# Kernel tuning notes

Measured on AMD Instinct MI355X. Metric: run time of the kernel, lower is better.

## Reference

```python
import jax, jax.numpy as jnp
import numpy as np

B, I, H = 4096, 1024, 1024


def setup_inputs() -> dict:
    key = jax.random.key(0)
    ks = jax.random.split(key, 22)
    def n(k, shape, scale=1.0):
        return jax.random.normal(k, shape, dtype=jnp.float32) * scale
    s = 0.02  # small init for weights to keep gates in sensitive range
    return {
        "x": n(ks[0], (B, I)),
        "h": n(ks[1], (B, H)),
        "c": n(ks[2], (B, H)),
        "W_ii_w": n(ks[3], (H, I), s), "W_ii_b": n(ks[4], (H,), s),
        "W_hi_w": n(ks[5], (H, H), s), "W_hi_b": n(ks[6], (H,), s),
        "W_ci":   n(ks[7], (H,), s),
        "W_if_w": n(ks[8], (H, I), s), "W_if_b": n(ks[9], (H,), s),
        "W_hf_w": n(ks[10], (H, H), s), "W_hf_b": n(ks[11], (H,), s),
        "W_cf":   n(ks[12], (H,), s),
        "W_ig_w": n(ks[13], (H, I), s), "W_ig_b": n(ks[14], (H,), s),
        "W_hg_w": n(ks[15], (H, H), s), "W_hg_b": n(ks[16], (H,), s),
        "W_io_w": n(ks[17], (H, I), s), "W_io_b": n(ks[18], (H,), s),
        "W_ho_w": n(ks[19], (H, H), s), "W_ho_b": n(ks[20], (H,), s),
        "W_co":   n(ks[21], (H,), s),
    }


def reference(x, h, c,
              W_ii_w, W_ii_b, W_hi_w, W_hi_b, W_ci,
              W_if_w, W_if_b, W_hf_w, W_hf_b, W_cf,
              W_ig_w, W_ig_b, W_hg_w, W_hg_b,
              W_io_w, W_io_b, W_ho_w, W_ho_b, W_co):
    # Fuse the 4 input projections and 4 hidden projections into single GEMMs.
    # Weight layout matches torch nn.Linear: y = x @ W.T + b
    Wx = jnp.concatenate([W_ii_w, W_if_w, W_ig_w, W_io_w], axis=0)  # [4H, I]
    Wh = jnp.concatenate([W_hi_w, W_hf_w, W_hg_w, W_ho_w], axis=0)  # [4H, H]
    bx = jnp.concatenate([W_ii_b, W_if_b, W_ig_b, W_io_b])          # [4H]
    bh = jnp.concatenate([W_hi_b, W_hf_b, W_hg_b, W_ho_b])          # [4H]
    z = x @ Wx.T + h @ Wh.T + (bx + bh)  # [B, 4H]
    zi, zf, zg, zo = jnp.split(z, 4, axis=-1)
    i = jax.nn.sigmoid(zi + W_ci * c)
    f = jax.nn.sigmoid(zf + W_cf * c)
    g = jnp.tanh(zg)
    c_next = f * c + i * g
    o = jax.nn.sigmoid(zo + W_co * c_next)
    h_next = o * jnp.tanh(c_next)
    return (h_next, c_next)
```

## Files before the change

kernel.cpp:

```cpp
#include <hip/hip_runtime.h>
#include <hip/hip_bf16.h>

#define BD 4096
#define ID 1024
#define HD 1024
#define KD 2048
#define ND 4096

typedef __attribute__((ext_vector_type(8))) __bf16 bf16x8;
typedef __attribute__((ext_vector_type(4))) float f32x4;

static __device__ __forceinline__ unsigned short f2bf(float f) {
  union { float f; unsigned u; } v; v.f = f;
  unsigned u = v.u;
  unsigned r = u + 0x7fffu + ((u >> 16) & 1u);
  return (unsigned short)(r >> 16);
}
static __device__ __forceinline__ float bf2f(unsigned short s) {
  union { unsigned u; float f; } v; v.u = ((unsigned)s) << 16;
  return v.f;
}

static __device__ __forceinline__ void gload_lds16(const void* g, void* l) {
  __builtin_amdgcn_global_load_lds(
      (const __attribute__((address_space(1))) void*)g,
      (__attribute__((address_space(3))) void*)l, 16, 0, 0);
}

static __device__ __forceinline__ float fast_sigmoid(float x) {
  return 1.0f / (1.0f + __expf(-x));
}
static __device__ __forceinline__ float fast_tanh(float x) {
  float t = __expf(-2.0f * fabsf(x));
  float r = (1.0f - t) / (1.0f + t);
  return copysignf(r, x);
}

__global__ void pack_AB(const float* __restrict__ x, const float* __restrict__ h,
                        const float* __restrict__ wxi, const float* __restrict__ wxf,
                        const float* __restrict__ wxg, const float* __restrict__ wxo,
                        const float* __restrict__ whi, const float* __restrict__ whf,
                        const float* __restrict__ whg, const float* __restrict__ who,
                        unsigned short* __restrict__ A, unsigned short* __restrict__ Bm) {
  if (blockIdx.x < 8192) {
    int idx = blockIdx.x * blockDim.x + threadIdx.x;
    int e = idx << 2;
    int b = e >> 11;
    int k = e & 2047;
    const float* src = (k < ID) ? (x + (size_t)b * ID + k)
                                : (h + (size_t)b * HD + (k - ID));
    float4 v = *reinterpret_cast<const float4*>(src);
    ushort4 o;
    o.x = f2bf(v.x); o.y = f2bf(v.y); o.z = f2bf(v.z); o.w = f2bf(v.w);
    *reinterpret_cast<ushort4*>(A + e) = o;
  } else {
    int idx = (blockIdx.x - 8192) * blockDim.x + threadIdx.x;
    int e = idx << 2;
    int n = e >> 11;
    int k = e & 2047;
    int g = n >> 10, r = n & 1023;
    const float* src;
    if (k < ID) {
      src = (g == 0) ? wxi : (g == 1) ? wxf : (g == 2) ? wxg : wxo;
      src += (size_t)r * ID + k;
    } else {
      src = (g == 0) ? whi : (g == 1) ? whf : (g == 2) ? whg : who;
      src += (size_t)r * HD + (k - ID);
    }
    float4 v = *reinterpret_cast<const float4*>(src);
    ushort4 o;
    o.x = f2bf(v.x); o.y = f2bf(v.y); o.z = f2bf(v.z); o.w = f2bf(v.w);
    *reinterpret_cast<ushort4*>(Bm + e) = o;
  }
}

__global__ __launch_bounds__(512, 2) void gemm_bf16(
    const unsigned short* __restrict__ A,
    const unsigned short* __restrict__ Bm,
    unsigned short* __restrict__ Z) {
  __shared__ __attribute__((aligned(16))) unsigned short lds[65536];

  const int tid  = threadIdx.x;
  const int lane = tid & 63;
  const int w    = tid >> 6;
  const int wr   = w >> 2;
  const int wc   = w & 3;

  const int bid = blockIdx.x;
  const int swz = (bid & 7) * 32 + (bid >> 3);
  const int m0  = (swz >> 4) * 256;
  const int n0  = (swz & 15) * 256;

  f32x4 acc[8][4];
#pragma unroll
  for (int i = 0; i < 8; ++i)
#pragma unroll
    for (int j = 0; j < 4; ++j)
      acc[i][j] = (f32x4){0.f, 0.f, 0.f, 0.f};

  const int sw  = lane & 7;
  const int rA0 = (wr * 128 + (lane & 15)) * 64;
  const int rB0 = (wc * 64  + (lane & 15)) * 64;
  const int offk0 = (((lane >> 4)    ) ^ sw) * 8;
  const int offk1 = (((lane >> 4) + 4) ^ sw) * 8;

  unsigned short* ldsA = lds;
  unsigned short* ldsB = lds + 32768;

  auto stage = [&](int buf, int kt) {
#pragma unroll
    for (int j = 0; j < 4; ++j) {
      int ci  = j * 512 + tid;
      int row = ci >> 3;
      int sc  = (ci & 7) ^ (row & 7);
      const unsigned short* gA = A  + (size_t)(m0 + row) * KD + kt + sc * 8;
      const unsigned short* gB = Bm + (size_t)(n0 + row) * KD + kt + sc * 8;
      unsigned short* lA = ldsA + buf * 16384 + (j * 512 + (tid & ~63)) * 8;
      unsigned short* lB = ldsB + buf * 16384 + (j * 512 + (tid & ~63)) * 8;
      gload_lds16(gA, lA);
      gload_lds16(gB, lB);
    }
  };

  stage(0, 0);

  for (int T = 0; T < 32; ++T) {
    const int buf = T & 1;
    const unsigned short* pA = ldsA + buf * 16384;
    const unsigned short* pB = ldsB + buf * 16384;

    asm volatile("s_waitcnt vmcnt(0)" ::: "memory");
    __builtin_amdgcn_s_barrier();
    __builtin_amdgcn_sched_barrier(0);

    bf16x8 bfr[4][2];
#pragma unroll
    for (int ni = 0; ni < 4; ++ni) {
      bfr[ni][0] = *(const bf16x8*)(pB + rB0 + ni * 1024 + offk0);
      bfr[ni][1] = *(const bf16x8*)(pB + rB0 + ni * 1024 + offk1);
    }

    if (T < 31) stage(buf ^ 1, (T + 1) * 64);
    __builtin_amdgcn_sched_barrier(0);

#pragma unroll
    for (int p = 0; p < 4; ++p) {
      bf16x8 af[2][2];
#pragma unroll
      for (int i = 0; i < 2; ++i) {
        af[i][0] = *(const bf16x8*)(pA + rA0 + (2 * p + i) * 1024 + offk0);
        af[i][1] = *(const bf16x8*)(pA + rA0 + (2 * p + i) * 1024 + offk1);
      }
      __builtin_amdgcn_s_setprio(1);
#pragma unroll
      for (int i = 0; i < 2; ++i)
#pragma unroll
        for (int ni = 0; ni < 4; ++ni)
#pragma unroll
          for (int kk = 0; kk < 2; ++kk)
            acc[2 * p + i][ni] = __builtin_amdgcn_mfma_f32_16x16x32_bf16(
                af[i][kk], bfr[ni][kk], acc[2 * p + i][ni], 0, 0, 0);
      __builtin_amdgcn_s_setprio(0);
      __builtin_amdgcn_s_barrier();
    }
  }

  const int col0 = n0 + wc * 64 + (lane & 15);
  const int row0 = m0 + wr * 128 + (lane >> 4) * 4;
#pragma unroll
  for (int mi = 0; mi < 8; ++mi)
#pragma unroll
    for (int ni = 0; ni < 4; ++ni)
#pragma unroll
      for (int q = 0; q < 4; ++q)
        Z[(size_t)(row0 + mi * 16 + q) * ND + col0 + ni * 16] =
            f2bf(acc[mi][ni][q]);
}

__global__ void lstm_cell(const unsigned short* __restrict__ Z,
                          const float* __restrict__ c,
                          const float* __restrict__ bxi, const float* __restrict__ bhi,
                          const float* __restrict__ bxf, const float* __restrict__ bhf,
                          const float* __restrict__ bxg, const float* __restrict__ bhg,
                          const float* __restrict__ bxo, const float* __restrict__ bho,
                          const float* __restrict__ pci, const float* __restrict__ pcf,
                          const float* __restrict__ pco,
                          float* __restrict__ out) {
  int idx = blockIdx.x * blockDim.x + threadIdx.x;
  int e = idx << 2;
  int b = e >> 10;
  int r = e & 1023;
  const size_t zrow = (size_t)b * ND;

  ushort4 zi4 = *(const ushort4*)&Z[zrow + r];
  ushort4 zf4 = *(const ushort4*)&Z[zrow + 1024 + r];
  ushort4 zg4 = *(const ushort4*)&Z[zrow + 2048 + r];
  ushort4 zo4 = *(const ushort4*)&Z[zrow + 3072 + r];
  float4 c4   = *(const float4*)&c[e];
  float4 vbxi = *(const float4*)&bxi[r];
  float4 vbhi = *(const float4*)&bhi[r];
  float4 vbxf = *(const float4*)&bxf[r];
  float4 vbhf = *(const float4*)&bhf[r];
  float4 vbxg = *(const float4*)&bxg[r];
  float4 vbhg = *(const float4*)&bhg[r];
  float4 vbxo = *(const float4*)&bxo[r];
  float4 vbho = *(const float4*)&bho[r];
  float4 vpci = *(const float4*)&pci[r];
  float4 vpcf = *(const float4*)&pcf[r];
  float4 vpco = *(const float4*)&pco[r];

  unsigned short ziu[4] = {zi4.x, zi4.y, zi4.z, zi4.w};
  unsigned short zfu[4] = {zf4.x, zf4.y, zf4.z, zf4.w};
  unsigned short zgu[4] = {zg4.x, zg4.y, zg4.z, zg4.w};
  unsigned short zou[4] = {zo4.x, zo4.y, zo4.z, zo4.w};
  float cc[4]  = {c4.x, c4.y, c4.z, c4.w};
  float bi_[4] = {vbxi.x + vbhi.x, vbxi.y + vbhi.y, vbxi.z + vbhi.z, vbxi.w + vbhi.w};
  float bf_[4] = {vbxf.x + vbhf.x, vbxf.y + vbhf.y, vbxf.z + vbhf.z, vbxf.w + vbhf.w};
  float bg_[4] = {vbxg.x + vbhg.x, vbxg.y + vbhg.y, vbxg.z + vbhg.z, vbxg.w + vbhg.w};
  float bo_[4] = {vbxo.x + vbho.x, vbxo.y + vbho.y, vbxo.z + vbho.z, vbxo.w + vbho.w};
  float pi_[4] = {vpci.x, vpci.y, vpci.z, vpci.w};
  float pf_[4] = {vpcf.x, vpcf.y, vpcf.z, vpcf.w};
  float po_[4] = {vpco.x, vpco.y, vpco.z, vpco.w};

  float hn[4], cn[4];
#pragma unroll
  for (int j = 0; j < 4; ++j) {
    float vi = bf2f(ziu[j]) + bi_[j] + pi_[j] * cc[j];
    float vf = bf2f(zfu[j]) + bf_[j] + pf_[j] * cc[j];
    float vg = bf2f(zgu[j]) + bg_[j];
    float vo = bf2f(zou[j]) + bo_[j];
    float ig = fast_sigmoid(vi);
    float fg = fast_sigmoid(vf);
    float gg = fast_tanh(vg);
    float cnext = fg * cc[j] + ig * gg;
    float og = fast_sigmoid(vo + po_[j] * cnext);
    cn[j] = cnext;
    hn[j] = og * fast_tanh(cnext);
  }
  float4 ho = {hn[0], hn[1], hn[2], hn[3]};
  float4 co = {cn[0], cn[1], cn[2], cn[3]};
  *(float4*)&out[e] = ho;
  *(float4*)&out[(size_t)BD * HD + e] = co;
}

extern "C" void kernel_launch(void* const* d_in, const int* in_sizes, int n_in,
                              void* d_out, int out_size, void* d_ws, size_t ws_size,
                              hipStream_t stream) {
  const float* x      = (const float*)d_in[0];
  const float* h      = (const float*)d_in[1];
  const float* c      = (const float*)d_in[2];
  const float* W_ii_w = (const float*)d_in[3];
  const float* W_ii_b = (const float*)d_in[4];
  const float* W_hi_w = (const float*)d_in[5];
  const float* W_hi_b = (const float*)d_in[6];
  const float* W_ci   = (const float*)d_in[7];
  const float* W_if_w = (const float*)d_in[8];
  const float* W_if_b = (const float*)d_in[9];
  const float* W_hf_w = (const float*)d_in[10];
  const float* W_hf_b = (const float*)d_in[11];
  const float* W_cf   = (const float*)d_in[12];
  const float* W_ig_w = (const float*)d_in[13];
  const float* W_ig_b = (const float*)d_in[14];
  const float* W_hg_w = (const float*)d_in[15];
  const float* W_hg_b = (const float*)d_in[16];
  const float* W_io_w = (const float*)d_in[17];
  const float* W_io_b = (const float*)d_in[18];
  const float* W_ho_w = (const float*)d_in[19];
  const float* W_ho_b = (const float*)d_in[20];
  const float* W_co   = (const float*)d_in[21];

  unsigned short* Apack = (unsigned short*)d_ws;
  unsigned short* Bpack = Apack + (size_t)BD * KD;
  unsigned short* Zbuf  = Bpack + (size_t)ND * KD;
  float* out = (float*)d_out;

  pack_AB<<<dim3(16384), dim3(256), 0, stream>>>(
      x, h, W_ii_w, W_if_w, W_ig_w, W_io_w, W_hi_w, W_hf_w, W_hg_w, W_ho_w,
      Apack, Bpack);
  gemm_bf16<<<dim3(256), dim3(512), 0, stream>>>(Apack, Bpack, Zbuf);
  lstm_cell<<<dim3(4096), dim3(256), 0, stream>>>(Zbuf, c,
      W_ii_b, W_hi_b, W_if_b, W_hf_b, W_ig_b, W_hg_b, W_io_b, W_ho_b,
      W_ci, W_cf, W_co, out);
}
```

Measured before the change: 234.9 us.

## Split A-tile staging per sub-phase and wait on partial vmcnt counts

Global-to-LDS loads for the next A tile are now split into four row chunks, one issued per sub-phase p of the compute loop, while B is issued at p==0. Each sub-phase waits only on the vmcnt needed for its A chunk, replacing the full vmcnt(0) drain at the top of each K step. The last K step is peeled into an epilogue with a decreasing vmcnt countdown. The goal is to spread memory issue across the MFMA work and shorten stalls. The trade-off is more barriers, plus correctness that depends on exact per-thread load counts and the LDS layout matching the reader indexing.

Result: no change. 234.1 us (-0.3%).

```diff
diff --git a/kernel.cpp b/kernel.cpp
--- a/kernel.cpp
+++ b/kernel.cpp
@@ -107,50 +107,62 @@
   unsigned short* ldsA = lds;
   unsigned short* ldsB = lds + 32768;
 
-  auto stage = [&](int buf, int kt) {
-#pragma unroll
-    for (int j = 0; j < 4; ++j) {
-      int ci  = j * 512 + tid;
+  auto stageB = [&](int buf, int kt) {
+#pragma unroll
+    for (int q = 0; q < 4; ++q) {
+      int ci  = q * 512 + tid;
       int row = ci >> 3;
       int sc  = (ci & 7) ^ (row & 7);
-      const unsigned short* gA = A  + (size_t)(m0 + row) * KD + kt + sc * 8;
-      const unsigned short* gB = Bm + (size_t)(n0 + row) * KD + kt + sc * 8;
-      unsigned short* lA = ldsA + buf * 16384 + (j * 512 + (tid & ~63)) * 8;
-      unsigned short* lB = ldsB + buf * 16384 + (j * 512 + (tid & ~63)) * 8;
-      gload_lds16(gA, lA);
-      gload_lds16(gB, lB);
+      gload_lds16(Bm + (size_t)(n0 + row) * KD + kt + sc * 8,
+                  ldsB + buf * 16384 + (q * 512 + w * 64) * 8);
     }
   };
-
-  stage(0, 0);
-
-  for (int T = 0; T < 32; ++T) {
+  auto stageA = [&](int buf, int kt, int p) {
+    int half = tid >> 8;
+    int idx  = tid & 255;
+    int row  = half * 128 + p * 32 + (idx >> 3);
+    int sc   = (idx & 7) ^ ((idx >> 3) & 7);
+    gload_lds16(A + (size_t)(m0 + row) * KD + kt + sc * 8,
+                ldsA + buf * 16384 + (half * 1024 + p * 256 + (w & 3) * 64) * 8);
+  };
+
+  stageB(0, 0);
+  stageA(0, 0, 0);
+  stageA(0, 0, 1);
+  stageA(0, 0, 2);
+  stageA(0, 0, 3);
+
+  bf16x8 bfr[4][2];
+
+  for (int T = 0; T < 31; ++T) {
     const int buf = T & 1;
     const unsigned short* pA = ldsA + buf * 16384;
     const unsigned short* pB = ldsB + buf * 16384;
-
-    asm volatile("s_waitcnt vmcnt(0)" ::: "memory");
+    const int ktn = (T + 1) * 64;
+
+    asm volatile("s_waitcnt vmcnt(3)" ::: "memory");
     __builtin_amdgcn_s_barrier();
     __builtin_amdgcn_sched_barrier(0);
 
-    bf16x8 bfr[4][2];
-#pragma unroll
-    for (int ni = 0; ni < 4; ++ni) {
-      bfr[ni][0] = *(const bf16x8*)(pB + rB0 + ni * 1024 + offk0);
-      bfr[ni][1] = *(const bf16x8*)(pB + rB0 + ni * 1024 + offk1);
-    }
-
-    if (T < 31) stage(buf ^ 1, (T + 1) * 64);
-    __builtin_amdgcn_sched_barrier(0);
-
 #pragma unroll
     for (int p = 0; p < 4; ++p) {
+      if (p == 0) {
+#pragma unroll
+        for (int ni = 0; ni < 4; ++ni) {
+          bfr[ni][0] = *(const bf16x8*)(pB + rB0 + ni * 1024 + offk0);
+          bfr[ni][1] = *(const bf16x8*)(pB + rB0 + ni * 1024 + offk1);
+        }
+      }
       bf16x8 af[2][2];
 #pragma unroll
       for (int i = 0; i < 2; ++i) {
         af[i][0] = *(const bf16x8*)(pA + rA0 + (2 * p + i) * 1024 + offk0);
         af[i][1] = *(const bf16x8*)(pA + rA0 + (2 * p + i) * 1024 + offk1);
       }
+      if (p == 0) { stageB(buf ^ 1, ktn); stageA(buf ^ 1, ktn, 0); }
+      else        { stageA(buf ^ 1, ktn, p); }
+      __builtin_amdgcn_sched_barrier(0);
+
       __builtin_amdgcn_s_setprio(1);
 #pragma unroll
       for (int i = 0; i < 2; ++i)
@@ -161,7 +173,51 @@
             acc[2 * p + i][ni] = __builtin_amdgcn_mfma_f32_16x16x32_bf16(
                 af[i][kk], bfr[ni][kk], acc[2 * p + i][ni], 0, 0, 0);
       __builtin_amdgcn_s_setprio(0);
-      __builtin_amdgcn_s_barrier();
+
+      if (p < 3) {
+        asm volatile("s_waitcnt vmcnt(7)" ::: "memory");
+        __builtin_amdgcn_s_barrier();
+      }
+    }
+  }
+
+  {
+    const unsigned short* pA = ldsA + 16384;
+    const unsigned short* pB = ldsB + 16384;
+
+    asm volatile("s_waitcnt vmcnt(3)" ::: "memory");
+    __builtin_amdgcn_s_barrier();
+    __builtin_amdgcn_sched_barrier(0);
+
+#pragma unroll
+    for (int p = 0; p < 4; ++p) {
+      if (p == 0) {
+#pragma unroll
+        for (int ni = 0; ni < 4; ++ni) {
+          bfr[ni][0] = *(const bf16x8*)(pB + rB0 + ni * 1024 + offk0);
+          bfr[ni][1] = *(const bf16x8*)(pB + rB0 + ni * 1024 + offk1);
+        }
+      }
+      bf16x8 af[2][2];
+#pragma unroll
+      for (int i = 0; i < 2; ++i) {
+        af[i][0] = *(const bf16x8*)(pA + rA0 + (2 * p + i) * 1024 + offk0);
+        af[i][1] = *(const bf16x8*)(pA + rA0 + (2 * p + i) * 1024 + offk1);
+      }
+      __builtin_amdgcn_s_setprio(1);
+#pragma unroll
+      for (int i = 0; i < 2; ++i)
+#pragma unroll
+        for (int ni = 0; ni < 4; ++ni)
+#pragma unroll
+          for (int kk = 0; kk < 2; ++kk)
+            acc[2 * p + i][ni] = __builtin_amdgcn_mfma_f32_16x16x32_bf16(
+                af[i][kk], bfr[ni][kk], acc[2 * p + i][ni], 0, 0, 0);
+      __builtin_amdgcn_s_setprio(0);
+
+      if (p == 0) { asm volatile("s_waitcnt vmcnt(2)" ::: "memory"); __builtin_amdgcn_s_barrier(); }
+      if (p == 1) { asm volatile("s_waitcnt vmcnt(1)" ::: "memory"); __builtin_amdgcn_s_barrier(); }
+      if (p == 2) { asm volatile("s_waitcnt vmcnt(0)" ::: "memory"); __builtin_amdgcn_s_barrier(); }
     }
   }
 
```

## Fuse LSTM cell epilogue into GEMM with gate-interleaved weight rows

Applied to the files above, without the earlier changes.

Weight rows are repacked so the four gates of each hidden unit sit in adjacent output columns. This lets each GEMM tile compute the LSTM cell directly in its epilogue through an LDS-staged Z tile, removing the bf16 Z round trip through global memory and the separate elementwise launch. The A/B global-to-LDS staging is also split across the inner p-steps to spread load issue, and the last per-iteration barrier is dropped. The epilogue does scalar, less-coalesced loads of c and stores of the outputs and needs slightly more LDS.

After: 220.6 us. 6.1% less time.

```diff
diff --git a/kernel.cpp b/kernel.cpp
--- a/kernel.cpp
+++ b/kernel.cpp
@@ -58,7 +58,7 @@
     int e = idx << 2;
     int n = e >> 11;
     int k = e & 2047;
-    int g = n >> 10, r = n & 1023;
+    int g = n & 3, r = n >> 2;
     const float* src;
     if (k < ID) {
       src = (g == 0) ? wxi : (g == 1) ? wxf : (g == 2) ? wxg : wxo;
@@ -74,11 +74,18 @@
   }
 }
 
-__global__ __launch_bounds__(512, 2) void gemm_bf16(
+__global__ __launch_bounds__(512, 2) void gemm_lstm(
     const unsigned short* __restrict__ A,
     const unsigned short* __restrict__ Bm,
-    unsigned short* __restrict__ Z) {
-  __shared__ __attribute__((aligned(16))) unsigned short lds[65536];
+    const float* __restrict__ c,
+    const float* __restrict__ bxi, const float* __restrict__ bhi,
+    const float* __restrict__ bxf, const float* __restrict__ bhf,
+    const float* __restrict__ bxg, const float* __restrict__ bhg,
+    const float* __restrict__ bxo, const float* __restrict__ bho,
+    const float* __restrict__ pci, const float* __restrict__ pcf,
+    const float* __restrict__ pco,
+    float* __restrict__ out) {
+  __shared__ __attribute__((aligned(16))) unsigned short lds[67584];
 
   const int tid  = threadIdx.x;
   const int lane = tid & 63;
@@ -107,50 +114,65 @@
   unsigned short* ldsA = lds;
   unsigned short* ldsB = lds + 32768;
 
-  auto stage = [&](int buf, int kt) {
-#pragma unroll
-    for (int j = 0; j < 4; ++j) {
-      int ci  = j * 512 + tid;
+  auto stageB = [&](int buf, int kt) {
+#pragma unroll
+    for (int q = 0; q < 4; ++q) {
+      int ci  = q * 512 + tid;
       int row = ci >> 3;
       int sc  = (ci & 7) ^ (row & 7);
-      const unsigned short* gA = A  + (size_t)(m0 + row) * KD + kt + sc * 8;
-      const unsigned short* gB = Bm + (size_t)(n0 + row) * KD + kt + sc * 8;
-      unsigned short* lA = ldsA + buf * 16384 + (j * 512 + (tid & ~63)) * 8;
-      unsigned short* lB = ldsB + buf * 16384 + (j * 512 + (tid & ~63)) * 8;
-      gload_lds16(gA, lA);
-      gload_lds16(gB, lB);
+      gload_lds16(Bm + (size_t)(n0 + row) * KD + kt + sc * 8,
+                  ldsB + buf * 16384 + (q * 512 + w * 64) * 8);
     }
   };
-
-  stage(0, 0);
+  auto stageA = [&](int buf, int kt, int p) {
+    int half = tid >> 8;
+    int idx  = tid & 255;
+    int row  = half * 128 + p * 32 + (idx >> 3);
+    int sc   = (idx & 7) ^ ((idx >> 3) & 7);
+    gload_lds16(A + (size_t)(m0 + row) * KD + kt + sc * 8,
+                ldsA + buf * 16384 + (half * 1024 + p * 256 + (w & 3) * 64) * 8);
+  };
+
+  stageB(0, 0);
+  stageA(0, 0, 0);
+  stageA(0, 0, 1);
+  stageA(0, 0, 2);
+  stageA(0, 0, 3);
+
+  bf16x8 bfr[4][2];
 
   for (int T = 0; T < 32; ++T) {
     const int buf = T & 1;
     const unsigned short* pA = ldsA + buf * 16384;
     const unsigned short* pB = ldsB + buf * 16384;
+    const int ktn = (T + 1) * 64;
 
     asm volatile("s_waitcnt vmcnt(0)" ::: "memory");
     __builtin_amdgcn_s_barrier();
     __builtin_amdgcn_sched_barrier(0);
 
-    bf16x8 bfr[4][2];
-#pragma unroll
-    for (int ni = 0; ni < 4; ++ni) {
-      bfr[ni][0] = *(const bf16x8*)(pB + rB0 + ni * 1024 + offk0);
-      bfr[ni][1] = *(const bf16x8*)(pB + rB0 + ni * 1024 + offk1);
-    }
-
-    if (T < 31) stage(buf ^ 1, (T + 1) * 64);
-    __builtin_amdgcn_sched_barrier(0);
-
 #pragma unroll
     for (int p = 0; p < 4; ++p) {
+      if (p == 0) {
+#pragma unroll
+        for (int ni = 0; ni < 4; ++ni) {
+          bfr[ni][0] = *(const bf16x8*)(pB + rB0 + ni * 1024 + offk0);
+          bfr[ni][1] = *(const bf16x8*)(pB + rB0 + ni * 1024 + offk1);
+        }
+      }
       bf16x8 af[2][2];
 #pragma unroll
       for (int i = 0; i < 2; ++i) {
         af[i][0] = *(const bf16x8*)(pA + rA0 + (2 * p + i) * 1024 + offk0);
         af[i][1] = *(const bf16x8*)(pA + rA0 + (2 * p + i) * 1024 + offk1);
       }
+      if (T < 31) {
+        if (p == 0)      { stageB(buf ^ 1, ktn); }
+        else if (p == 1) { stageA(buf ^ 1, ktn, 0); stageA(buf ^ 1, ktn, 1); }
+        else if (p == 2) { stageA(buf ^ 1, ktn, 2); stageA(buf ^ 1, ktn, 3); }
+      }
+      __builtin_amdgcn_sched_barrier(0);
+
       __builtin_amdgcn_s_setprio(1);
 #pragma unroll
       for (int i = 0; i < 2; ++i)
@@ -161,86 +183,55 @@
             acc[2 * p + i][ni] = __builtin_amdgcn_mfma_f32_16x16x32_bf16(
                 af[i][kk], bfr[ni][kk], acc[2 * p + i][ni], 0, 0, 0);
       __builtin_amdgcn_s_setprio(0);
-      __builtin_amdgcn_s_barrier();
+
+      if (p < 3) __builtin_amdgcn_s_barrier();
     }
   }
 
-  const int col0 = n0 + wc * 64 + (lane & 15);
-  const int row0 = m0 + wr * 128 + (lane >> 4) * 4;
+  unsigned short* zl = lds;
+  __builtin_amdgcn_s_barrier();
 #pragma unroll
   for (int mi = 0; mi < 8; ++mi)
 #pragma unroll
-    for (int ni = 0; ni < 4; ++ni)
-#pragma unroll
-      for (int q = 0; q < 4; ++q)
-        Z[(size_t)(row0 + mi * 16 + q) * ND + col0 + ni * 16] =
-            f2bf(acc[mi][ni][q]);
-}
-
-__global__ void lstm_cell(const unsigned short* __restrict__ Z,
-                          const float* __restrict__ c,
-                          const float* __restrict__ bxi, const float* __restrict__ bhi,
-                          const float* __restrict__ bxf, const float* __restrict__ bhf,
-                          const float* __restrict__ bxg, const float* __restrict__ bhg,
-                          const float* __restrict__ bxo, const float* __restrict__ bho,
-                          const float* __restrict__ pci, const float* __restrict__ pcf,
-                          const float* __restrict__ pco,
-                          float* __restrict__ out) {
-  int idx = blockIdx.x * blockDim.x + threadIdx.x;
-  int e = idx << 2;
-  int b = e >> 10;
-  int r = e & 1023;
-  const size_t zrow = (size_t)b * ND;
-
-  ushort4 zi4 = *(const ushort4*)&Z[zrow + r];
-  ushort4 zf4 = *(const ushort4*)&Z[zrow + 1024 + r];
-  ushort4 zg4 = *(const ushort4*)&Z[zrow + 2048 + r];
-  ushort4 zo4 = *(const ushort4*)&Z[zrow + 3072 + r];
-  float4 c4   = *(const float4*)&c[e];
-  float4 vbxi = *(const float4*)&bxi[r];
-  float4 vbhi = *(const float4*)&bhi[r];
-  float4 vbxf = *(const float4*)&bxf[r];
-  float4 vbhf = *(const float4*)&bhf[r];
-  float4 vbxg = *(const float4*)&bxg[r];
-  float4 vbhg = *(const float4*)&bhg[r];
-  float4 vbxo = *(const float4*)&bxo[r];
-  float4 vbho = *(const float4*)&bho[r];
-  float4 vpci = *(const float4*)&pci[r];
-  float4 vpcf = *(const float4*)&pcf[r];
-  float4 vpco = *(const float4*)&pco[r];
-
-  unsigned short ziu[4] = {zi4.x, zi4.y, zi4.z, zi4.w};
-  unsigned short zfu[4] = {zf4.x, zf4.y, zf4.z, zf4.w};
-  unsigned short zgu[4] = {zg4.x, zg4.y, zg4.z, zg4.w};
-  unsigned short zou[4] = {zo4.x, zo4.y, zo4.z, zo4.w};
-  float cc[4]  = {c4.x, c4.y, c4.z, c4.w};
-  float bi_[4] = {vbxi.x + vbhi.x, vbxi.y + vbhi.y, vbxi.z + vbhi.z, vbxi.w + vbhi.w};
-  float bf_[4] = {vbxf.x + vbhf.x, vbxf.y + vbhf.y, vbxf.z + vbhf.z, vbxf.w + vbhf.w};
-  float bg_[4] = {vbxg.x + vbhg.x, vbxg.y + vbhg.y, vbxg.z + vbhg.z, vbxg.w + vbhg.w};
-  float bo_[4] = {vbxo.x + vbho.x, vbxo.y + vbho.y, vbxo.z + vbho.z, vbxo.w + vbho.w};
-  float pi_[4] = {vpci.x, vpci.y, vpci.z, vpci.w};
-  float pf_[4] = {vpcf.x, vpcf.y, vpcf.z, vpcf.w};
-  float po_[4] = {vpco.x, vpco.y, vpco.z, vpco.w};
-
-  float hn[4], cn[4];
-#pragma unroll
-  for (int j = 0; j < 4; ++j) {
-    float vi = bf2f(ziu[j]) + bi_[j] + pi_[j] * cc[j];
-    float vf = bf2f(zfu[j]) + bf_[j] + pf_[j] * cc[j];
-    float vg = bf2f(zgu[j]) + bg_[j];
-    float vo = bf2f(zou[j]) + bo_[j];
-    float ig = fast_sigmoid(vi);
-    float fg = fast_sigmoid(vf);
-    float gg = fast_tanh(vg);
-    float cnext = fg * cc[j] + ig * gg;
-    float og = fast_sigmoid(vo + po_[j] * cnext);
-    cn[j] = cnext;
-    hn[j] = og * fast_tanh(cnext);
+    for (int ni = 0; ni < 4; ++ni) {
+      const int cl = wc * 64 + ni * 16 + (lane & 15);
+#pragma unroll
+      for (int q = 0; q < 4; ++q) {
+        const int rl = wr * 128 + (lane >> 4) * 4 + mi * 16 + q;
+        zl[rl * 264 + cl] = f2bf(acc[mi][ni][q]);
+      }
+    }
+  __builtin_amdgcn_s_barrier();
+
+  {
+    const int r_loc = tid & 63;
+    const int rg    = (n0 >> 2) + r_loc;
+    const float bi_ = bxi[rg] + bhi[rg];
+    const float bf_ = bxf[rg] + bhf[rg];
+    const float bg_ = bxg[rg] + bhg[rg];
+    const float bo_ = bxo[rg] + bho[rg];
+    const float pi_ = pci[rg];
+    const float pf_ = pcf[rg];
+    const float po_ = pco[rg];
+#pragma unroll 4
+    for (int it = 0; it < 32; ++it) {
+      const int rl  = (tid >> 6) + it * 8;
+      const int row = m0 + rl;
+      ushort4 zv = *(const ushort4*)&zl[rl * 264 + r_loc * 4];
+      float cc = c[(size_t)row * HD + rg];
+      float vi = bf2f(zv.x) + bi_ + pi_ * cc;
+      float vf = bf2f(zv.y) + bf_ + pf_ * cc;
+      float vg = bf2f(zv.z) + bg_;
+      float vo = bf2f(zv.w) + bo_;
+      float ig = fast_sigmoid(vi);
+      float fg = fast_sigmoid(vf);
+      float gg = fast_tanh(vg);
+      float cnext = fg * cc + ig * gg;
+      float og = fast_sigmoid(vo + po_ * cnext);
+      out[(size_t)row * HD + rg] = og * fast_tanh(cnext);
+      out[(size_t)BD * HD + (size_t)row * HD + rg] = cnext;
+    }
   }
-  float4 ho = {hn[0], hn[1], hn[2], hn[3]};
-  float4 co = {cn[0], cn[1], cn[2], cn[3]};
-  *(float4*)&out[e] = ho;
-  *(float4*)&out[(size_t)BD * HD + e] = co;
 }
 
 extern "C" void kernel_launch(void* const* d_in, const int* in_sizes, int n_in,
@@ -271,14 +262,13 @@
 
   unsigned short* Apack = (unsigned short*)d_ws;
   unsigned short* Bpack = Apack + (size_t)BD * KD;
-  unsigned short* Zbuf  = Bpack + (size_t)ND * KD;
   float* out = (float*)d_out;
 
   pack_AB<<<dim3(16384), dim3(256), 0, stream>>>(
       x, h, W_ii_w, W_if_w, W_ig_w, W_io_w, W_hi_w, W_hf_w, W_hg_w, W_ho_w,
       Apack, Bpack);
-  gemm_bf16<<<dim3(256), dim3(512), 0, stream>>>(Apack, Bpack, Zbuf);
-  lstm_cell<<<dim3(4096), dim3(256), 0, stream>>>(Zbuf, c,
+  gemm_lstm<<<dim3(256), dim3(512), 0, stream>>>(
+      Apack, Bpack, c,
       W_ii_b, W_hi_b, W_if_b, W_hf_b, W_ig_b, W_hg_b, W_io_b, W_ho_b,
       W_ci, W_cf, W_co, out);
 }
```
